# Optimization experiments

Measured on AMD Instinct MI355X. Metric: run time of the kernel, lower is better.

Reference implementation:

```python
import jax, jax.numpy as jnp
import numpy as np

B, S = 512, 256
NUM_LOC, NUM_USERS, D = 50000, 10000, 256
MAX_RECENT = 5
DQ = D // 4            # user/hour/weekday embed dim
TEMP = 3 * DQ          # temporal feature size
H2 = D // 2            # scorer hidden
NEG = -1e9


def setup_inputs() -> dict:
    key = jax.random.key(0)
    ks = jax.random.split(key, 25)
    p = lambda i, shape: jax.random.normal(ks[i], shape, jnp.float32) * 0.02

    locations = jax.random.randint(ks[0], (B, S), 0, NUM_LOC)
    users = jax.random.randint(ks[1], (B, S), 0, NUM_USERS)
    weekdays = jax.random.randint(ks[2], (B, S), 0, 8)
    start_mins = jax.random.randint(ks[3], (B, S), 0, 1440)
    lengths = jax.random.randint(ks[4], (B,), 1, S + 1)  # ragged valid lengths
    mask = jnp.arange(S)[None, :] < lengths[:, None]     # (B,S) bool prefix mask

    return {
        "locations": locations, "users": users, "weekdays": weekdays,
        "start_mins": start_mins, "mask": mask,
        # embedding tables (padding_idx=0 row zeroed, matching torch init)
        "loc_table": p(5, (NUM_LOC, D)).at[0].set(0.0),
        "user_table": p(6, (NUM_USERS, DQ)).at[0].set(0.0),
        "hour_table": p(7, (25, DQ)).at[0].set(0.0),
        "wd_table": p(8, (8, DQ)).at[0].set(0.0),
        # LSTM (PyTorch layout: gates i,f,g,o stacked)
        "W_ih": p(9, (4 * D, D + TEMP)), "W_hh": p(10, (4 * D, D)),
        "b_ih": p(11, (4 * D,)), "b_hh": p(12, (4 * D,)),
        # recent-location scorer MLP
        "sc_W1": p(13, (H2, D + 2)), "sc_b1": p(14, (H2,)),
        "sc_W2": p(15, (1, H2)), "sc_b2": p(16, (1,)),
        # new-location predictor MLP (dropout is identity in eval)
        "np_W1": p(17, (D, D)), "np_b1": p(18, (D,)),
        "np_W2": p(19, (NUM_LOC, D)), "np_b2": p(20, (NUM_LOC,)),
        # mix predictor
        "mx_W": p(21, (1, D)), "mx_b": p(22, (1,)),
    }


def _forward(locations, users, weekdays, start_mins, mask,
             loc_table, user_table, hour_table, wd_table,
             W_ih, W_hh, b_ih, b_hh,
             sc_W1, sc_b1, sc_W2, sc_b2,
             np_W1, np_b1, np_W2, np_b2, mx_W, mx_b):
    gelu = lambda x: jax.nn.gelu(x, approximate=False)  # torch nn.GELU default

    hours = jnp.clip(start_mins // 60, 0, 24)
    temporal = jnp.concatenate(
        [user_table[users], hour_table[hours], wd_table[weekdays]], axis=-1)
    x = jnp.concatenate([loc_table[locations], temporal], axis=-1)  # (B,S,D+TEMP)

    # --- LSTM over time via scan (PyTorch gate order i,f,g,o) ---
    def step(carry, xt):
        h, c = carry
        g = xt @ W_ih.T + b_ih + h @ W_hh.T + b_hh
        i, f, gg, o = jnp.split(g, 4, axis=-1)
        c = jax.nn.sigmoid(f) * c + jax.nn.sigmoid(i) * jnp.tanh(gg)
        h = jax.nn.sigmoid(o) * jnp.tanh(c)
        return (h, c), h

    h0 = jnp.zeros((x.shape[0], D), x.dtype)
    _, outs = jax.lax.scan(step, (h0, h0), jnp.swapaxes(x, 0, 1))
    output = jnp.swapaxes(outs, 0, 1)  # (B,S,D)

    seq_lens = mask.sum(axis=1).astype(jnp.int32) - 1  # last valid index
    bids = jnp.arange(output.shape[0])
    context = output[bids, seq_lens]                   # (B,D)

    # --- vectorized ragged recent-location scoring (j=0 is last visit) ---
    j = jnp.arange(MAX_RECENT)
    idx = seq_lens[:, None] - j[None, :]               # (B,R) indices from end
    valid = idx >= 0                                   # j < seq_len_b
    idxc = jnp.clip(idx, 0, S - 1)
    bidx = bids[:, None]
    rlocs = locations[bidx, idxc]                      # (B,R)
    rtimes = start_mins[bidx, idxc]
    cur_time = start_mins[bids, seq_lens][:, None]
    tdiff = ((cur_time - rtimes).astype(jnp.float32) / 1440.0)[..., None]
    pos = jnp.broadcast_to(j.astype(jnp.float32), rlocs.shape)[..., None]
    feats = jnp.concatenate([loc_table[rlocs], tdiff, pos], axis=-1)  # (B,R,D+2)
    scores = (gelu(feats @ sc_W1.T + sc_b1) @ sc_W2.T + sc_b2)[..., 0]  # (B,R)

    # drop entry jj if some newer valid entry j' < jj has the same location.
    eq = rlocs[:, :, None] == rlocs[:, None, :]        # (B, jj, j')
    newer = (j[:, None] > j[None, :])[None]            # jj > j'
    dup = jnp.any(eq & newer & valid[:, None, :], axis=-1)
    keep = valid & ~dup
    scatter_locs = jnp.where(keep, rlocs, NUM_LOC)     # out-of-range -> dropped

    recent_logits = jnp.full((rlocs.shape[0], NUM_LOC), NEG, jnp.float32)
    recent_logits = recent_logits.at[bidx, scatter_locs].set(scores, mode='drop')

    new_logits = gelu(context @ np_W1.T + np_b1) @ np_W2.T + np_b2  # (B,NUM_LOC)
    mix = jax.nn.sigmoid(context @ mx_W.T + mx_b) * 0.9 + 0.05     # (B,1)
    return mix * recent_logits + (1.0 - mix) * new_logits


def reference(locations, users, weekdays, start_mins, mask,
              loc_table, user_table, hour_table, wd_table,
              W_ih, W_hh, b_ih, b_hh,
              sc_W1, sc_b1, sc_W2, sc_b2,
              np_W1, np_b1, np_W2, np_b2, mx_W, mx_b):
    return _forward(locations, users, weekdays, start_mins, mask,
                    loc_table, user_table, hour_table, wd_table,
                    W_ih, W_hh, b_ih, b_hh,
                    sc_W1, sc_b1, sc_W2, sc_b2,
                    np_W1, np_b1, np_W2, np_b2, mx_W, mx_b)
```

## Files before the change

### kernel.cpp

```cpp
#include <hip/hip_runtime.h>
#include <hip/hip_bf16.h>
#include <math.h>

#define B_ 512
#define S_ 256
#define D_ 256
#define NLOC 50000
#define KX 448
#define G4 1024
#define NEGV -1000000000.0f

typedef __attribute__((ext_vector_type(8))) short short8;
typedef __attribute__((ext_vector_type(4))) float f32x4;

__device__ __forceinline__ float sigmoidf_(float x){ return 1.0f/(1.0f+expf(-x)); }
__device__ __forceinline__ float geluf_(float x){ return 0.5f*x*(1.0f+erff(x*0.70710678118654752f)); }
__device__ __forceinline__ unsigned short f2bf_(float x){
  __hip_bfloat16 h = __float2bfloat16(x);
  return *(unsigned short*)&h;
}
__device__ __forceinline__ float bf2f_(unsigned short u){
  __hip_bfloat16 h = *(__hip_bfloat16*)&u;
  return __bfloat162float(h);
}

__global__ void k_init(unsigned short* hbf, float* c, int* flag){
  int i = blockIdx.x*256 + threadIdx.x;
  if (i < B_*D_){ hbf[i]=0; c[i]=0.f; }
  if (i==0) *flag = 0;
}

__global__ void k_detect(const unsigned char* m, int* flag){
  int i = blockIdx.x*256 + threadIdx.x;
  if ((i & 1) && i < B_*S_ && m[i]) atomicOr(flag, 1);
}

__global__ void k_seqlen(const void* mp, const int* flag, int* slens){
  int b = blockIdx.x*256 + threadIdx.x;
  if (b >= B_) return;
  int cnt = 0;
  if (*flag){
    const unsigned char* m = (const unsigned char*)mp;
    for (int s=0;s<S_;s++) cnt += (m[b*S_+s] != 0);
  } else {
    const int* m = (const int*)mp;
    for (int s=0;s<S_;s++) cnt += (m[b*S_+s] != 0);
  }
  slens[b] = cnt - 1;
}

__global__ void k_buildw(const float* wih, const float* whh, const float* bih,
                         const float* bhh, unsigned short* Wihbf,
                         unsigned short* Whhbf, float* btot){
  int i = blockIdx.x*256 + threadIdx.x;
  if (i < G4*KX) Wihbf[i] = f2bf_(wih[i]);
  if (i < G4*D_) Whhbf[i] = f2bf_(whh[i]);
  if (i < G4) btot[i] = bih[i] + bhh[i];
}

__global__ __launch_bounds__(256) void k_gx(
    const int* __restrict__ loc, const int* __restrict__ usr,
    const int* __restrict__ wdy, const int* __restrict__ sm,
    const float* __restrict__ loct, const float* __restrict__ usert,
    const float* __restrict__ hourt, const float* __restrict__ wdt,
    const unsigned short* __restrict__ Wihbf, const float* __restrict__ btot,
    unsigned short* __restrict__ Gx){
  __shared__ unsigned short As[128][40];
  int tid = threadIdx.x;
  int n0 = blockIdx.x*128, m0 = blockIdx.y*128;
  int w = tid>>6, lane = tid&63;
  int quad = lane>>4, l16 = lane&15;
  int mw = (w>>1)*64, nw = (w&1)*64;
  f32x4 acc[4][4] = {};
  int r0 = tid>>2, seg = tid&3;
  for (int kt=0; kt<14; kt++){
    int k0 = kt*32;
    int kc = k0 + seg*8;
    #pragma unroll
    for (int rr=0; rr<2; rr++){
      int r = r0 + rr*64;
      int row = m0 + r;
      const float* src;
      if (kc < 256)      src = loct  + (size_t)loc[row]*256 + kc;
      else if (kc < 320) src = usert + (size_t)usr[row]*64 + (kc-256);
      else if (kc < 384) { int s = sm[row]; int hh = s/60; if (hh>24) hh=24; if (hh<0) hh=0;
                           src = hourt + (size_t)hh*64 + (kc-320); }
      else               src = wdt   + (size_t)wdy[row]*64 + (kc-384);
      float4 v0 = *(const float4*)(src);
      float4 v1 = *(const float4*)(src+4);
      short8 pk;
      pk[0]=f2bf_(v0.x); pk[1]=f2bf_(v0.y); pk[2]=f2bf_(v0.z); pk[3]=f2bf_(v0.w);
      pk[4]=f2bf_(v1.x); pk[5]=f2bf_(v1.y); pk[6]=f2bf_(v1.z); pk[7]=f2bf_(v1.w);
      *(short8*)&As[r][seg*8] = pk;
    }
    __syncthreads();
    short8 bfrag[4], afrag[4];
    #pragma unroll
    for (int nt=0; nt<4; nt++)
      bfrag[nt] = *(const short8*)(Wihbf + (size_t)(n0+nw+nt*16+l16)*KX + k0 + quad*8);
    #pragma unroll
    for (int mt=0; mt<4; mt++)
      afrag[mt] = *(const short8*)&As[mw+mt*16+l16][quad*8];
    #pragma unroll
    for (int mt=0; mt<4; mt++)
      #pragma unroll
      for (int nt=0; nt<4; nt++)
        acc[mt][nt] = __builtin_amdgcn_mfma_f32_16x16x32_bf16(afrag[mt], bfrag[nt], acc[mt][nt], 0, 0, 0);
    __syncthreads();
  }
  #pragma unroll
  for (int nt=0; nt<4; nt++){
    int col = n0 + nw + nt*16 + l16;
    float bv = btot[col];
    #pragma unroll
    for (int mt=0; mt<4; mt++){
      #pragma unroll
      for (int i=0; i<4; i++){
        int row = m0 + mw + mt*16 + quad*4 + i;
        Gx[(size_t)row*G4 + col] = f2bf_(acc[mt][nt][i] + bv);
      }
    }
  }
}

__global__ __launch_bounds__(256) void k_step(int t,
    const unsigned short* __restrict__ Gx, const unsigned short* __restrict__ Whhbf,
    const unsigned short* __restrict__ hin, unsigned short* __restrict__ hout,
    float* __restrict__ c, float* __restrict__ ctx, const int* __restrict__ slens){
  int tid = threadIdx.x;
  int w = tid>>6, lane = tid&63;
  int quad = lane>>4, l16 = lane&15;
  int m0 = blockIdx.x*16;
  int d0 = (blockIdx.y*4 + w)*16;
  f32x4 acc[4] = {};
  #pragma unroll
  for (int kt=0; kt<8; kt++){
    int k0 = kt*32;
    short8 af = *(const short8*)(hin + (size_t)(m0+l16)*D_ + k0 + quad*8);
    #pragma unroll
    for (int q=0; q<4; q++){
      short8 bf = *(const short8*)(Whhbf + (size_t)(q*D_ + d0 + l16)*D_ + k0 + quad*8);
      acc[q] = __builtin_amdgcn_mfma_f32_16x16x32_bf16(af, bf, acc[q], 0, 0, 0);
    }
  }
  int d = d0 + l16;
  #pragma unroll
  for (int i=0; i<4; i++){
    int b = m0 + quad*4 + i;
    size_t gbase = ((size_t)b*S_ + t)*G4;
    float gi = acc[0][i] + bf2f_(Gx[gbase + d]);
    float gf = acc[1][i] + bf2f_(Gx[gbase + 256 + d]);
    float gg = acc[2][i] + bf2f_(Gx[gbase + 512 + d]);
    float go = acc[3][i] + bf2f_(Gx[gbase + 768 + d]);
    size_t ci = (size_t)b*D_ + d;
    float cold = c[ci];
    float cn = sigmoidf_(gf)*cold + sigmoidf_(gi)*tanhf(gg);
    float hn = sigmoidf_(go)*tanhf(cn);
    c[ci] = cn;
    hout[ci] = f2bf_(hn);
    if (t == slens[b]) ctx[ci] = hn;
  }
}

__global__ void k_post1(const float* __restrict__ ctx, const float* __restrict__ W1,
                        const float* __restrict__ b1, const float* __restrict__ mxW,
                        const float* __restrict__ mxb, float* newhid, float* mixv){
  __shared__ float cs[256];
  __shared__ float red[256];
  int b = blockIdx.x, tid = threadIdx.x;
  cs[tid] = ctx[(size_t)b*D_ + tid];
  __syncthreads();
  float a = b1[tid];
  const float* wr = W1 + (size_t)tid*D_;
  for (int k=0; k<D_; k++) a += cs[k]*wr[k];
  newhid[(size_t)b*D_ + tid] = geluf_(a);
  red[tid] = cs[tid]*mxW[tid];
  __syncthreads();
  for (int s=128; s>0; s>>=1){ if (tid<s) red[tid]+=red[tid+s]; __syncthreads(); }
  if (tid==0) mixv[b] = sigmoidf_(red[0]+mxb[0])*0.9f + 0.05f;
}

__global__ void k_recent(const int* __restrict__ loc, const int* __restrict__ sm,
                         const int* __restrict__ slens, const float* __restrict__ loct,
                         const float* __restrict__ W1, const float* __restrict__ b1,
                         const float* __restrict__ W2, const float* __restrict__ b2,
                         float* scores, int* rlocs, int* keep){
  __shared__ int rl[5], vs[5];
  __shared__ float td[5];
  __shared__ float red[128];
  int b = blockIdx.x, tid = threadIdx.x;
  int sl = slens[b];
  if (tid < 5){
    int idx = sl - tid;
    int v = idx >= 0;
    int ic = v ? idx : 0;
    rl[tid] = loc[b*S_ + ic];
    vs[tid] = v;
    int cur = sm[b*S_ + sl];
    td[tid] = (float)(cur - sm[b*S_ + ic]) * (1.0f/1440.0f);
  }
  __syncthreads();
  for (int j=0; j<5; j++){
    const float* lrow = loct + (size_t)rl[j]*D_;
    const float* wr = W1 + (size_t)tid*258;
    float a = b1[tid];
    for (int k=0; k<D_; k++) a += lrow[k]*wr[k];
    a += td[j]*wr[256] + (float)j*wr[257];
    red[tid] = geluf_(a)*W2[tid];
    __syncthreads();
    for (int s=64; s>0; s>>=1){ if (tid<s) red[tid]+=red[tid+s]; __syncthreads(); }
    if (tid==0) scores[b*5+j] = red[0] + b2[0];
    __syncthreads();
  }
  if (tid==0){
    for (int j=0; j<5; j++){
      int dup = 0;
      for (int k=0; k<j; k++) dup |= (rl[j]==rl[k]) && vs[k];
      keep[b*5+j] = vs[j] && !dup;
      rlocs[b*5+j] = rl[j];
    }
  }
}

__global__ __launch_bounds__(256) void k_final(const float* __restrict__ newhid,
    const float* __restrict__ W2, const float* __restrict__ b2,
    const float* __restrict__ mixv, float* __restrict__ out){
  __shared__ float Hs[16][256];
  __shared__ float Wl[64][65];
  int tid = threadIdx.x;
  int l0 = blockIdx.x*64, b0 = blockIdx.y*16;
  int ll = tid & 63, bq = tid >> 6;
  #pragma unroll
  for (int r=0; r<16; r++) Hs[r][tid] = newhid[(size_t)(b0+r)*D_ + tid];
  float acc[4] = {0.f,0.f,0.f,0.f};
  for (int kt=0; kt<4; kt++){
    int k0 = kt*64;
    __syncthreads();
    #pragma unroll
    for (int r=0; r<4; r++){
      int row = 4*r + bq;
      int l = l0 + row;
      Wl[row][ll] = (l < NLOC) ? W2[(size_t)l*D_ + k0 + ll] : 0.f;
    }
    __syncthreads();
    #pragma unroll
    for (int kk=0; kk<64; kk++){
      float wv = Wl[ll][kk];
      #pragma unroll
      for (int bi=0; bi<4; bi++) acc[bi] += wv * Hs[bq*4+bi][k0+kk];
    }
  }
  int l = l0 + ll;
  if (l < NLOC){
    float bias = b2[l];
    #pragma unroll
    for (int bi=0; bi<4; bi++){
      int b = b0 + bq*4 + bi;
      float mx = mixv[b];
      out[(size_t)b*NLOC + l] = mx*NEGV + (1.0f-mx)*(acc[bi] + bias);
    }
  }
}

__global__ void k_scatter(const float* __restrict__ newhid, const float* __restrict__ W2,
                          const float* __restrict__ b2, const float* __restrict__ mixv,
                          const float* __restrict__ scores, const int* __restrict__ rlocs,
                          const int* __restrict__ keep, float* out){
  int b = blockIdx.x, lane = threadIdx.x;
  float mx = mixv[b];
  for (int j=0; j<5; j++){
    if (!keep[b*5+j]) continue;
    int rl = rlocs[b*5+j];
    const float* wr = W2 + (size_t)rl*D_;
    const float* hr = newhid + (size_t)b*D_;
    float a = 0.f;
    #pragma unroll
    for (int q=0; q<4; q++){ int k = lane + 64*q; a += hr[k]*wr[k]; }
    #pragma unroll
    for (int off=32; off>0; off>>=1) a += __shfl_xor(a, off, 64);
    if (lane==0)
      out[(size_t)b*NLOC + rl] = mx*scores[b*5+j] + (1.0f-mx)*(a + b2[rl]);
  }
}

extern "C" void kernel_launch(void* const* d_in, const int* in_sizes, int n_in,
                              void* d_out, int out_size, void* d_ws, size_t ws_size,
                              hipStream_t stream){
  const int* locations   = (const int*)d_in[0];
  const int* users       = (const int*)d_in[1];
  const int* weekdays    = (const int*)d_in[2];
  const int* start_mins  = (const int*)d_in[3];
  const void* mask       = d_in[4];
  const float* loc_table = (const float*)d_in[5];
  const float* user_table= (const float*)d_in[6];
  const float* hour_table= (const float*)d_in[7];
  const float* wd_table  = (const float*)d_in[8];
  const float* W_ih      = (const float*)d_in[9];
  const float* W_hh      = (const float*)d_in[10];
  const float* b_ih      = (const float*)d_in[11];
  const float* b_hh      = (const float*)d_in[12];
  const float* sc_W1     = (const float*)d_in[13];
  const float* sc_b1     = (const float*)d_in[14];
  const float* sc_W2     = (const float*)d_in[15];
  const float* sc_b2     = (const float*)d_in[16];
  const float* np_W1     = (const float*)d_in[17];
  const float* np_b1     = (const float*)d_in[18];
  const float* np_W2     = (const float*)d_in[19];
  const float* np_b2     = (const float*)d_in[20];
  const float* mx_W      = (const float*)d_in[21];
  const float* mx_b      = (const float*)d_in[22];
  float* out = (float*)d_out;

  char* w = (char*)d_ws;
  size_t o = 0;
  auto alloc = [&](size_t bytes)->void*{ void* p = w + o; o += (bytes + 255) & ~(size_t)255; return p; };
  unsigned short* Gx    = (unsigned short*)alloc((size_t)B_*S_*G4*sizeof(short));
  unsigned short* Wihbf = (unsigned short*)alloc((size_t)G4*KX*sizeof(short));
  unsigned short* Whhbf = (unsigned short*)alloc((size_t)G4*D_*sizeof(short));
  float* btot   = (float*)alloc((size_t)G4*sizeof(float));
  unsigned short* hbf0 = (unsigned short*)alloc((size_t)B_*D_*sizeof(short));
  unsigned short* hbf1 = (unsigned short*)alloc((size_t)B_*D_*sizeof(short));
  float* cbuf   = (float*)alloc((size_t)B_*D_*sizeof(float));
  float* ctx    = (float*)alloc((size_t)B_*D_*sizeof(float));
  float* newhid = (float*)alloc((size_t)B_*D_*sizeof(float));
  float* mixv   = (float*)alloc((size_t)B_*sizeof(float));
  float* scores = (float*)alloc((size_t)B_*5*sizeof(float));
  int*   slens  = (int*)alloc((size_t)B_*sizeof(int));
  int*   rlocs  = (int*)alloc((size_t)B_*5*sizeof(int));
  int*   keep   = (int*)alloc((size_t)B_*5*sizeof(int));
  int*   flag   = (int*)alloc(sizeof(int));

  k_init<<<512, 256, 0, stream>>>(hbf0, cbuf, flag);
  k_detect<<<512, 256, 0, stream>>>((const unsigned char*)mask, flag);
  k_seqlen<<<2, 256, 0, stream>>>(mask, flag, slens);
  k_buildw<<<1792, 256, 0, stream>>>(W_ih, W_hh, b_ih, b_hh, Wihbf, Whhbf, btot);
  k_gx<<<dim3(8,1024), 256, 0, stream>>>(locations, users, weekdays, start_mins,
                                         loc_table, user_table, hour_table, wd_table,
                                         Wihbf, btot, Gx);
  for (int t=0; t<S_; t++){
    unsigned short* hin  = (t & 1) ? hbf1 : hbf0;
    unsigned short* hout = (t & 1) ? hbf0 : hbf1;
    k_step<<<dim3(32,4), 256, 0, stream>>>(t, Gx, Whhbf, hin, hout, cbuf, ctx, slens);
  }
  k_post1<<<512, 256, 0, stream>>>(ctx, np_W1, np_b1, mx_W, mx_b, newhid, mixv);
  k_recent<<<512, 128, 0, stream>>>(locations, start_mins, slens, loc_table,
                                    sc_W1, sc_b1, sc_W2, sc_b2, scores, rlocs, keep);
  k_final<<<dim3(782,32), 256, 0, stream>>>(newhid, np_W2, np_b2, mixv, out);
  k_scatter<<<512, 64, 0, stream>>>(newhid, np_W2, np_b2, mixv, scores, rlocs, keep, out);
}
```

Before: 3.562 ms.

## Fuse LSTM time loop into one persistent kernel with LDS-staged gate prefetch

Replaces 256 per-timestep kernel launches with a single persistent kernel of 32 blocks, each owning 16 batch rows for the whole sequence. Hidden state stays in LDS and cell state in registers, and half of W_hh is cached in registers. The next step's Gx slice is prefetched into LDS via global_load_lds double buffering, with Gx relaid out time-major so each step's slice is contiguous. It also switches to fast sigmoid/tanh intrinsics, which are slightly less accurate, and the whole recurrence now runs on only 32 CUs.

```diff
diff --git a/kernel.cpp b/kernel.cpp
--- a/kernel.cpp
+++ b/kernel.cpp
@@ -23,11 +23,21 @@
   __hip_bfloat16 h = *(__hip_bfloat16*)&u;
   return __bfloat162float(h);
 }
-
-__global__ void k_init(unsigned short* hbf, float* c, int* flag){
-  int i = blockIdx.x*256 + threadIdx.x;
-  if (i < B_*D_){ hbf[i]=0; c[i]=0.f; }
-  if (i==0) *flag = 0;
+__device__ __forceinline__ float fsig_(float x){
+  return __fdividef(1.0f, 1.0f + __expf(-x));
+}
+__device__ __forceinline__ float ftanh_(float x){
+  float xc = fminf(fmaxf(x, -15.0f), 15.0f);
+  float e = __expf(2.0f*xc);
+  return __fdividef(e - 1.0f, e + 1.0f);
+}
+__device__ __forceinline__ void gld_lds16_(const unsigned short* gsrc, unsigned short* ldst){
+  __builtin_amdgcn_global_load_lds((const __attribute__((address_space(1))) void*)gsrc,
+                                   (__attribute__((address_space(3))) void*)ldst, 16, 0, 0);
+}
+
+__global__ void k_init(int* flag){
+  if (blockIdx.x==0 && threadIdx.x==0) *flag = 0;
 }
 
 __global__ void k_detect(const unsigned char* m, int* flag){
@@ -117,48 +127,111 @@
       #pragma unroll
       for (int i=0; i<4; i++){
         int row = m0 + mw + mt*16 + quad*4 + i;
-        Gx[(size_t)row*G4 + col] = f2bf_(acc[mt][nt][i] + bv);
+        int bb = row >> 8, tt = row & 255;
+        Gx[((size_t)tt*B_ + bb)*G4 + col] = f2bf_(acc[mt][nt][i] + bv);
       }
     }
   }
 }
 
-__global__ __launch_bounds__(256) void k_step(int t,
-    const unsigned short* __restrict__ Gx, const unsigned short* __restrict__ Whhbf,
-    const unsigned short* __restrict__ hin, unsigned short* __restrict__ hout,
-    float* __restrict__ c, float* __restrict__ ctx, const int* __restrict__ slens){
+__global__ __launch_bounds__(512, 2) void k_lstm(
+    const unsigned short* __restrict__ Gx,
+    const unsigned short* __restrict__ Whhbf,
+    float* __restrict__ ctx, const int* __restrict__ slens){
+  __shared__ unsigned short h_s[16][264];
+  __shared__ unsigned short gx_s[2][16*1024];
   int tid = threadIdx.x;
-  int w = tid>>6, lane = tid&63;
-  int quad = lane>>4, l16 = lane&15;
-  int m0 = blockIdx.x*16;
-  int d0 = (blockIdx.y*4 + w)*16;
-  f32x4 acc[4] = {};
+  int w = tid >> 6, lane = tid & 63;
+  int quad = lane >> 4, l16 = lane & 15;
+  int b0 = blockIdx.x * 16;
+  int dw = w * 32;
+
+  for (int i = tid; i < 16*264; i += 512) ((unsigned short*)h_s)[i] = 0;
+
+  short8 bc[4][2][4];
   #pragma unroll
-  for (int kt=0; kt<8; kt++){
-    int k0 = kt*32;
-    short8 af = *(const short8*)(hin + (size_t)(m0+l16)*D_ + k0 + quad*8);
-    #pragma unroll
-    for (int q=0; q<4; q++){
-      short8 bf = *(const short8*)(Whhbf + (size_t)(q*D_ + d0 + l16)*D_ + k0 + quad*8);
-      acc[q] = __builtin_amdgcn_mfma_f32_16x16x32_bf16(af, bf, acc[q], 0, 0, 0);
-    }
-  }
-  int d = d0 + l16;
+  for (int q=0;q<4;q++)
+    #pragma unroll
+    for (int nt=0;nt<2;nt++)
+      #pragma unroll
+      for (int kt=0;kt<4;kt++)
+        bc[q][nt][kt] = *(const short8*)(Whhbf + (size_t)(q*256 + dw + nt*16 + l16)*256 + kt*32 + quad*8);
+
+  float cst[2][4] = {{0.f,0.f,0.f,0.f},{0.f,0.f,0.f,0.f}};
+  int slq[4];
   #pragma unroll
-  for (int i=0; i<4; i++){
-    int b = m0 + quad*4 + i;
-    size_t gbase = ((size_t)b*S_ + t)*G4;
-    float gi = acc[0][i] + bf2f_(Gx[gbase + d]);
-    float gf = acc[1][i] + bf2f_(Gx[gbase + 256 + d]);
-    float gg = acc[2][i] + bf2f_(Gx[gbase + 512 + d]);
-    float go = acc[3][i] + bf2f_(Gx[gbase + 768 + d]);
-    size_t ci = (size_t)b*D_ + d;
-    float cold = c[ci];
-    float cn = sigmoidf_(gf)*cold + sigmoidf_(gi)*tanhf(gg);
-    float hn = sigmoidf_(go)*tanhf(cn);
-    c[ci] = cn;
-    hout[ci] = f2bf_(hn);
-    if (t == slens[b]) ctx[ci] = hn;
+  for (int i=0;i<4;i++) slq[i] = slens[b0 + quad*4 + i];
+
+  {
+    const unsigned short* src = Gx + (size_t)b0*G4 + w*2048 + lane*8;
+    unsigned short* dst = &gx_s[0][w*2048];
+    #pragma unroll
+    for (int j=0;j<4;j++) gld_lds16_(src + j*512, dst + j*512);
+  }
+  __syncthreads();
+
+  for (int t=0; t<S_; t++){
+    int cur = t & 1;
+    int tn = (t < S_-1) ? t+1 : t;
+    {
+      const unsigned short* src = Gx + ((size_t)tn*B_ + b0)*G4 + w*2048 + lane*8;
+      unsigned short* dst = &gx_s[cur^1][w*2048];
+      #pragma unroll
+      for (int j=0;j<4;j++) gld_lds16_(src + j*512, dst + j*512);
+    }
+
+    f32x4 acc[4][2] = {};
+    #pragma unroll
+    for (int kt=0; kt<8; kt++){
+      short8 af = *(const short8*)&h_s[l16][kt*32 + quad*8];
+      #pragma unroll
+      for (int q=0;q<4;q++)
+        #pragma unroll
+        for (int nt=0;nt<2;nt++){
+          short8 bf;
+          if (kt < 4) bf = bc[q][nt][kt];
+          else        bf = *(const short8*)(Whhbf + (size_t)(q*256 + dw + nt*16 + l16)*256 + kt*32 + quad*8);
+          acc[q][nt] = __builtin_amdgcn_mfma_f32_16x16x32_bf16(af, bf, acc[q][nt], 0, 0, 0);
+        }
+    }
+
+    asm volatile("s_waitcnt lgkmcnt(0) vmcnt(4)" ::: "memory");
+    __builtin_amdgcn_sched_barrier(0);
+    __builtin_amdgcn_s_barrier();
+
+    const unsigned int* gxw = (const unsigned int*)&gx_s[cur][0];
+    int half = l16 & 1;
+    #pragma unroll
+    for (int nt=0;nt<2;nt++){
+      int d = dw + nt*16 + l16;
+      int dbase2 = (dw + nt*16) >> 1;
+      #pragma unroll
+      for (int i=0;i<4;i++){
+        int r = quad*4 + i;
+        int base = r*512 + dbase2 + (l16>>1);
+        unsigned int u0 = gxw[base];
+        unsigned int u1 = gxw[base + 128];
+        unsigned int u2 = gxw[base + 256];
+        unsigned int u3 = gxw[base + 384];
+        unsigned short s0 = half ? (unsigned short)(u0>>16) : (unsigned short)(u0&0xffff);
+        unsigned short s1 = half ? (unsigned short)(u1>>16) : (unsigned short)(u1&0xffff);
+        unsigned short s2 = half ? (unsigned short)(u2>>16) : (unsigned short)(u2&0xffff);
+        unsigned short s3 = half ? (unsigned short)(u3>>16) : (unsigned short)(u3&0xffff);
+        float gi = acc[0][nt][i] + bf2f_(s0);
+        float gf = acc[1][nt][i] + bf2f_(s1);
+        float gg = acc[2][nt][i] + bf2f_(s2);
+        float go = acc[3][nt][i] + bf2f_(s3);
+        float cn = fsig_(gf)*cst[nt][i] + fsig_(gi)*ftanh_(gg);
+        float hn = fsig_(go)*ftanh_(cn);
+        cst[nt][i] = cn;
+        h_s[r][d] = f2bf_(hn);
+        if (t == slq[i]) ctx[(size_t)(b0 + r)*D_ + d] = hn;
+      }
+    }
+
+    asm volatile("s_waitcnt lgkmcnt(0)" ::: "memory");
+    __builtin_amdgcn_sched_barrier(0);
+    __builtin_amdgcn_s_barrier();
   }
 }
 
@@ -225,7 +298,7 @@
 __global__ __launch_bounds__(256) void k_final(const float* __restrict__ newhid,
     const float* __restrict__ W2, const float* __restrict__ b2,
     const float* __restrict__ mixv, float* __restrict__ out){
-  __shared__ float Hs[16][256];
+  __shared__ float Hs[16][260];
   __shared__ float Wl[64][65];
   int tid = threadIdx.x;
   int l0 = blockIdx.x*64, b0 = blockIdx.y*16;
@@ -318,9 +391,6 @@
   unsigned short* Wihbf = (unsigned short*)alloc((size_t)G4*KX*sizeof(short));
   unsigned short* Whhbf = (unsigned short*)alloc((size_t)G4*D_*sizeof(short));
   float* btot   = (float*)alloc((size_t)G4*sizeof(float));
-  unsigned short* hbf0 = (unsigned short*)alloc((size_t)B_*D_*sizeof(short));
-  unsigned short* hbf1 = (unsigned short*)alloc((size_t)B_*D_*sizeof(short));
-  float* cbuf   = (float*)alloc((size_t)B_*D_*sizeof(float));
   float* ctx    = (float*)alloc((size_t)B_*D_*sizeof(float));
   float* newhid = (float*)alloc((size_t)B_*D_*sizeof(float));
   float* mixv   = (float*)alloc((size_t)B_*sizeof(float));
@@ -330,18 +400,14 @@
   int*   keep   = (int*)alloc((size_t)B_*5*sizeof(int));
   int*   flag   = (int*)alloc(sizeof(int));
 
-  k_init<<<512, 256, 0, stream>>>(hbf0, cbuf, flag);
+  k_init<<<1, 64, 0, stream>>>(flag);
   k_detect<<<512, 256, 0, stream>>>((const unsigned char*)mask, flag);
   k_seqlen<<<2, 256, 0, stream>>>(mask, flag, slens);
   k_buildw<<<1792, 256, 0, stream>>>(W_ih, W_hh, b_ih, b_hh, Wihbf, Whhbf, btot);
   k_gx<<<dim3(8,1024), 256, 0, stream>>>(locations, users, weekdays, start_mins,
                                          loc_table, user_table, hour_table, wd_table,
                                          Wihbf, btot, Gx);
-  for (int t=0; t<S_; t++){
-    unsigned short* hin  = (t & 1) ? hbf1 : hbf0;
-    unsigned short* hout = (t & 1) ? hbf0 : hbf1;
-    k_step<<<dim3(32,4), 256, 0, stream>>>(t, Gx, Whhbf, hin, hout, cbuf, ctx, slens);
-  }
+  k_lstm<<<32, 512, 0, stream>>>(Gx, Whhbf, ctx, slens);
   k_post1<<<512, 256, 0, stream>>>(ctx, np_W1, np_b1, mx_W, mx_b, newhid, mixv);
   k_recent<<<512, 128, 0, stream>>>(locations, start_mins, slens, loc_table,
                                     sc_W1, sc_b1, sc_W2, sc_b2, scores, rlocs, keep);
```

Result: no change. 3.534 ms (-0.8%).
